# Kernel tuning notes

Measured on AMD Instinct MI355X. Metric: run time of the kernel, lower is better.

Reference implementation:

```python
import jax, jax.numpy as jnp
import numpy as np
from jax import lax

B, S, F_IN, H = 64, 512, 128, 512

def setup_inputs() -> dict:
    key = jax.random.key(0)
    ks = jax.random.split(key, 7)
    s = 1.0 / np.sqrt(H)
    return {
        "inputs": jax.random.normal(ks[0], (B, S, F_IN), dtype=jnp.float32),
        "W_ih": jax.random.normal(ks[1], (4 * H, F_IN), dtype=jnp.float32) * s,
        "W_hh": jax.random.normal(ks[2], (4 * H, H), dtype=jnp.float32) * s,
        "b_ih": jax.random.normal(ks[3], (4 * H,), dtype=jnp.float32) * s,
        "b_hh": jax.random.normal(ks[4], (4 * H,), dtype=jnp.float32) * s,
        "W_out": jax.random.normal(ks[5], (F_IN, H), dtype=jnp.float32) * s,
        "b_out": jax.random.normal(ks[6], (F_IN,), dtype=jnp.float32) * s,
    }

def reference(inputs, W_ih, W_hh, b_ih, b_hh, W_out, b_out):
    # inputs: [B, S, F]. Inference path: y=None, future=0 -> scan over all S steps.
    b, seq, _ = inputs.shape
    h = W_hh.shape[1]
    # Precompute input-to-gate projections for all timesteps: [S, B, 4H]
    x_gates = jnp.einsum("bsf,gf->sbg", inputs, W_ih) + b_ih + b_hh

    def step(carry, xg):
        h_t, c_t = carry
        gates = xg + h_t @ W_hh.T  # [B, 4H]
        i_g, f_g, g_g, o_g = jnp.split(gates, 4, axis=-1)
        i_g = jax.nn.sigmoid(i_g)
        f_g = jax.nn.sigmoid(f_g)
        g_g = jnp.tanh(g_g)
        o_g = jax.nn.sigmoid(o_g)
        c_t = f_g * c_t + i_g * g_g
        h_t = o_g * jnp.tanh(c_t)
        out = h_t @ W_out.T + b_out  # [B, F]
        return (h_t, c_t), out

    h0 = jnp.zeros((b, h), dtype=inputs.dtype)
    c0 = jnp.zeros((b, h), dtype=inputs.dtype)
    _, outs = lax.scan(step, (h0, c0), x_gates)  # outs: [S, B, F]
    return jnp.transpose(outs, (1, 0, 2))  # [B, S, F]
```

## Files before the change

### kernel.cpp

```cpp
#include <hip/hip_runtime.h>

typedef float f32x4 __attribute__((ext_vector_type(4)));

namespace {
constexpr int Bn = 64, Sn = 512, Fn = 128, Hn = 512;
constexpr int NWG = 256, NTHR = 512;
constexpr int HXS = 644;
constexpr int PQS = 581;
constexpr int RING0 = 1024;
}

__device__ __forceinline__ float sigmoid_f(float v) {
    return 1.0f / (1.0f + __expf(-v));
}
__device__ __forceinline__ float tanh_f(float v) {
    v = fminf(fmaxf(v, -15.0f), 15.0f);
    const float e = __expf(-2.0f * v);
    return (1.0f - e) / (1.0f + e);
}

__global__ __launch_bounds__(NTHR, 2)
void lstm_persist(const float* __restrict__ x,
                  const float* __restrict__ Wih,
                  const float* __restrict__ Whh,
                  const float* __restrict__ bih,
                  const float* __restrict__ bhh,
                  const float* __restrict__ Wout,
                  const float* __restrict__ bout,
                  float* __restrict__ out,
                  float* __restrict__ ws)
{
    const int w = blockIdx.x, t = threadIdx.x;
    const int xcd = w & 7, wi = w >> 3;
    const int rw = 4 * xcd + (wi & 3);
    const int bw = wi >> 2;

    const int q  = t & 31;
    const int r4 = t >> 5;
    const int k0 = 20 * q;

    const int out_fi  = (t >> 1) & 3;
    const int out_bb  = (t >> 3) & 7;
    const int out_ksl = ((t >> 6) << 1) | (t & 1);

    __shared__ float hx[8][HXS];
    __shared__ float part[32 * PQS];
    __shared__ float opart[4][8][9];
    __shared__ float gb[64];
    __shared__ float cst[16][9];
    __shared__ float bo[4];

    f32x4 wreg[4][5];
#pragma unroll
    for (int i2 = 0; i2 < 4; ++i2) {
        const int r = 4 * r4 + i2;
        const int G = (r >> 4) * Hn + rw * 16 + (r & 15);
#pragma unroll
        for (int j = 0; j < 5; ++j) {
            const int kk = k0 + 4 * j;
            const float* p = (kk < Hn) ? (Whh + (size_t)G * Hn + kk)
                                       : (Wih + (size_t)G * Fn + (kk - Hn));
            asm volatile("global_load_dwordx4 %0, %1, off"
                         : "=v"(wreg[i2][j]) : "v"(p));
        }
    }
    asm volatile("s_waitcnt vmcnt(0)");

    if (t < 64) {
        const int G = (t >> 4) * Hn + rw * 16 + (t & 15);
        gb[t] = bih[G] + bhh[G];
    }
    if (t < 4) bo[t] = bout[rw * 4 + t];
    if (t < 128) cst[t >> 3][t & 7] = 0.0f;

    unsigned* const bar = (unsigned*)ws;
    float* const ring = ws + RING0;

    if (t < 128) {
        const int ul = t & 15, bb = (t >> 4) & 7;
        float* hdst = ring + (size_t)(Bn * Hn) +
                      (size_t)(8 * bw + bb) * Hn + (16 * rw + ul);
        const float z = 0.0f;
        asm volatile("global_store_dword %0, %1, off sc0 sc1"
                     :: "v"(hdst), "v"(z) : "memory");
    }
    asm volatile("s_waitcnt vmcnt(0)" ::: "memory");
    __syncthreads();
    if (t == 0) {
        unsigned* gcnt = bar + 32 * ((w >> 4) + 1);
        const unsigned old = atomicAdd(gcnt, 1u);
        if (old == 15u) atomicAdd(bar, 1u);
        int guard = 0;
        while (__hip_atomic_load(bar, __ATOMIC_RELAXED,
                                 __HIP_MEMORY_SCOPE_AGENT) < 16u) {
            __builtin_amdgcn_s_sleep(1);
            if (++guard > 100000) break;
        }
    }
    __syncthreads();

    for (int k = 0; k <= Sn; ++k) {
        const int slot = (k & 1) ^ 1;
        const float* hsrc = ring + (size_t)slot * (Bn * Hn) + (size_t)bw * 8 * Hn;
        f32x4 v0, v1;
        {
            const float* p0 = hsrc + 4 * t;
            const float* p1 = p0 + 2048;
            asm volatile(
                "global_load_dwordx4 %0, %2, off sc0 sc1\n\t"
                "global_load_dwordx4 %1, %3, off sc0 sc1\n\t"
                "s_waitcnt vmcnt(0)"
                : "=&v"(v0), "=&v"(v1)
                : "v"(p0), "v"(p1));
        }
        {
            int fi = t;
            *(f32x4*)&hx[fi >> 7][(fi & 127) * 4] = v0;
            fi = t + 512;
            *(f32x4*)&hx[fi >> 7][(fi & 127) * 4] = v1;
        }
        if (k < Sn && t < 256) {
            const int bb = t >> 5, f4 = (t & 31) * 4;
            const f32x4 v = *(const f32x4*)(x + (size_t)(8 * bw + bb) * Sn * Fn +
                                            (size_t)k * Fn + f4);
            *(f32x4*)&hx[bb][Hn + f4] = v;
        }
        __syncthreads();

        if (k < Sn) {
            float acc[4][8];
#pragma unroll
            for (int i2 = 0; i2 < 4; ++i2)
#pragma unroll
                for (int ib = 0; ib < 8; ++ib) acc[i2][ib] = 0.0f;
#pragma unroll
            for (int j = 0; j < 5; ++j) {
                f32x4 hv[4];
#pragma unroll
                for (int ib = 0; ib < 4; ++ib)
                    hv[ib] = *(const f32x4*)&hx[ib][k0 + 4 * j];
#pragma unroll
                for (int i2 = 0; i2 < 4; ++i2)
#pragma unroll
                    for (int ib = 0; ib < 4; ++ib)
                        acc[i2][ib] += wreg[i2][j].x * hv[ib].x + wreg[i2][j].y * hv[ib].y +
                                       wreg[i2][j].z * hv[ib].z + wreg[i2][j].w * hv[ib].w;
#pragma unroll
                for (int ib = 0; ib < 4; ++ib)
                    hv[ib] = *(const f32x4*)&hx[4 + ib][k0 + 4 * j];
#pragma unroll
                for (int i2 = 0; i2 < 4; ++i2)
#pragma unroll
                    for (int ib = 0; ib < 4; ++ib)
                        acc[i2][4 + ib] += wreg[i2][j].x * hv[ib].x + wreg[i2][j].y * hv[ib].y +
                                           wreg[i2][j].z * hv[ib].z + wreg[i2][j].w * hv[ib].w;
            }
#pragma unroll
            for (int i2 = 0; i2 < 4; ++i2)
#pragma unroll
                for (int ib = 0; ib < 8; ++ib)
                    part[q * PQS + (4 * r4 + i2) * 9 + ib] = acc[i2][ib];
        }

        if (k >= 1 && t < 256) {
            const float* wo = Wout + (size_t)(rw * 4 + out_fi) * Hn + out_ksl * 64;
            const float* hrow = &hx[out_bb][out_ksl * 64];
            float oa = 0.0f;
#pragma unroll
            for (int jj = 0; jj < 16; ++jj) {
                const f32x4 wv = *(const f32x4*)(wo + 4 * jj);
                const f32x4 hv = *(const f32x4*)(hrow + 4 * jj);
                oa += wv.x * hv.x + wv.y * hv.y + wv.z * hv.z + wv.w * hv.w;
            }
            opart[out_fi][out_bb][out_ksl] = oa;
        }
        __syncthreads();

        if (k < Sn && t < 128) {
            const int ul = t & 15, bb = (t >> 4) & 7;
            float g4[4];
#pragma unroll
            for (int gate = 0; gate < 4; ++gate) {
                const int r = gate * 16 + ul;
                float s = gb[r];
#pragma unroll
                for (int qq = 0; qq < 32; ++qq) s += part[qq * PQS + r * 9 + bb];
                g4[gate] = s;
            }
            const float ig = sigmoid_f(g4[0]);
            const float fg = sigmoid_f(g4[1]);
            const float gg = tanh_f(g4[2]);
            const float og = sigmoid_f(g4[3]);
            const float cn = fg * cst[ul][bb] + ig * gg;
            cst[ul][bb] = cn;
            const float hn = og * tanh_f(cn);
            float* hdst = ring + (size_t)(k & 1) * (Bn * Hn) +
                          (size_t)(8 * bw + bb) * Hn + (16 * rw + ul);
            asm volatile("global_store_dword %0, %1, off sc0 sc1"
                         :: "v"(hdst), "v"(hn) : "memory");
        } else if (k >= 1 && t >= 128 && t < 160) {
            const int fi = (t - 128) >> 3, bb = (t - 128) & 7;
            float s = bo[fi];
#pragma unroll
            for (int qq = 0; qq < 8; ++qq) s += opart[fi][bb][qq];
            out[(size_t)(8 * bw + bb) * Sn * Fn + (size_t)(k - 1) * Fn + rw * 4 + fi] = s;
        }

        if (k < Sn) {
            asm volatile("s_waitcnt vmcnt(0)" ::: "memory");
            __syncthreads();
            if (t == 0) {
                const unsigned gen = (unsigned)(k + 2);
                unsigned* gcnt = bar + 32 * ((w >> 4) + 1);
                const unsigned old = atomicAdd(gcnt, 1u);
                if (old == 16u * gen - 1u) atomicAdd(bar, 1u);
                const unsigned target = 16u * gen;
                int guard = 0;
                while (__hip_atomic_load(bar, __ATOMIC_RELAXED,
                                         __HIP_MEMORY_SCOPE_AGENT) < target) {
                    __builtin_amdgcn_s_sleep(1);
                    if (++guard > 100000) break;
                }
            }
            __syncthreads();
        }
    }
}

extern "C" void kernel_launch(void* const* d_in, const int* in_sizes, int n_in,
                              void* d_out, int out_size, void* d_ws, size_t ws_size,
                              hipStream_t stream) {
    (void)in_sizes; (void)n_in; (void)out_size; (void)ws_size;
    const float* x    = (const float*)d_in[0];
    const float* Wih  = (const float*)d_in[1];
    const float* Whh  = (const float*)d_in[2];
    const float* bih  = (const float*)d_in[3];
    const float* bhh  = (const float*)d_in[4];
    const float* Wout = (const float*)d_in[5];
    const float* bout = (const float*)d_in[6];
    float* out = (float*)d_out;
    float* wsp = (float*)d_ws;

    hipMemsetAsync(d_ws, 0, 4096, stream);

    lstm_persist<<<dim3(NWG), dim3(NTHR), 0, stream>>>(
        x, Wih, Whh, bih, bhh, Wout, bout, out, wsp);
}
```

Before: 9.596 ms.

## Repartition LSTM across 512 workgroups of 256 threads with 8 hidden units each

Doubles the persistent workgroup count to 512 and halves threads per block to 256, so each workgroup now owns 8 hidden units (32 gate rows) instead of 16. Per-step matvec, gate reduction, output projection and barrier group sizes are remapped to match. The aim is to spread the recurrent work across more CUs and cut per-workgroup serial work on each timestep. In exchange every workgroup still reloads the full h slice for its batch group, so global traffic rises, and the grid barrier must now gather twice as many arrivals.

```diff
diff --git a/kernel.cpp b/kernel.cpp
--- a/kernel.cpp
+++ b/kernel.cpp
@@ -4,9 +4,9 @@
 
 namespace {
 constexpr int Bn = 64, Sn = 512, Fn = 128, Hn = 512;
-constexpr int NWG = 256, NTHR = 512;
+constexpr int NWG = 512, NTHR = 256;
 constexpr int HXS = 644;
-constexpr int PQS = 581;
+constexpr int PQS = 293;
 constexpr int RING0 = 1024;
 }
 
@@ -31,30 +31,30 @@
                   float* __restrict__ ws)
 {
     const int w = blockIdx.x, t = threadIdx.x;
-    const int xcd = w & 7, wi = w >> 3;
-    const int rw = 4 * xcd + (wi & 3);
-    const int bw = wi >> 2;
+    const int xcd = w & 7, wj = w >> 3;
+    const int rw = 8 * xcd + (wj & 7);
+    const int bw = wj >> 3;
 
     const int q  = t & 31;
     const int r4 = t >> 5;
     const int k0 = 20 * q;
 
-    const int out_fi  = (t >> 1) & 3;
-    const int out_bb  = (t >> 3) & 7;
-    const int out_ksl = ((t >> 6) << 1) | (t & 1);
+    const int out_fi  = t & 1;
+    const int out_bb  = (t >> 1) & 7;
+    const int out_ksl = t >> 4;
 
     __shared__ float hx[8][HXS];
     __shared__ float part[32 * PQS];
-    __shared__ float opart[4][8][9];
-    __shared__ float gb[64];
-    __shared__ float cst[16][9];
-    __shared__ float bo[4];
+    __shared__ float opart[2][8][17];
+    __shared__ float gb[32];
+    __shared__ float cst[64];
+    __shared__ float bo[2];
 
     f32x4 wreg[4][5];
 #pragma unroll
     for (int i2 = 0; i2 < 4; ++i2) {
         const int r = 4 * r4 + i2;
-        const int G = (r >> 4) * Hn + rw * 16 + (r & 15);
+        const int G = (r >> 3) * Hn + 8 * rw + (r & 7);
 #pragma unroll
         for (int j = 0; j < 5; ++j) {
             const int kk = k0 + 4 * j;
@@ -66,20 +66,20 @@
     }
     asm volatile("s_waitcnt vmcnt(0)");
 
-    if (t < 64) {
-        const int G = (t >> 4) * Hn + rw * 16 + (t & 15);
+    if (t < 32) {
+        const int G = (t >> 3) * Hn + 8 * rw + (t & 7);
         gb[t] = bih[G] + bhh[G];
     }
-    if (t < 4) bo[t] = bout[rw * 4 + t];
-    if (t < 128) cst[t >> 3][t & 7] = 0.0f;
+    if (t < 2) bo[t] = bout[rw * 2 + t];
+    if (t < 64) cst[t] = 0.0f;
 
     unsigned* const bar = (unsigned*)ws;
     float* const ring = ws + RING0;
 
-    if (t < 128) {
-        const int ul = t & 15, bb = (t >> 4) & 7;
+    if (t < 64) {
+        const int u = t & 7, bb = t >> 3;
         float* hdst = ring + (size_t)(Bn * Hn) +
-                      (size_t)(8 * bw + bb) * Hn + (16 * rw + ul);
+                      (size_t)(8 * bw + bb) * Hn + (8 * rw + u);
         const float z = 0.0f;
         asm volatile("global_store_dword %0, %1, off sc0 sc1"
                      :: "v"(hdst), "v"(z) : "memory");
@@ -87,14 +87,14 @@
     asm volatile("s_waitcnt vmcnt(0)" ::: "memory");
     __syncthreads();
     if (t == 0) {
-        unsigned* gcnt = bar + 32 * ((w >> 4) + 1);
+        unsigned* gcnt = bar + 32 * ((w >> 5) + 1);
         const unsigned old = atomicAdd(gcnt, 1u);
-        if (old == 15u) atomicAdd(bar, 1u);
+        if (old == 31u) atomicAdd(bar, 1u);
         int guard = 0;
         while (__hip_atomic_load(bar, __ATOMIC_RELAXED,
                                  __HIP_MEMORY_SCOPE_AGENT) < 16u) {
             __builtin_amdgcn_s_sleep(1);
-            if (++guard > 100000) break;
+            if (++guard > 200000) break;
         }
     }
     __syncthreads();
@@ -102,24 +102,32 @@
     for (int k = 0; k <= Sn; ++k) {
         const int slot = (k & 1) ^ 1;
         const float* hsrc = ring + (size_t)slot * (Bn * Hn) + (size_t)bw * 8 * Hn;
-        f32x4 v0, v1;
+        f32x4 v0, v1, v2, v3;
         {
             const float* p0 = hsrc + 4 * t;
-            const float* p1 = p0 + 2048;
+            const float* p1 = p0 + 1024;
+            const float* p2 = p0 + 2048;
+            const float* p3 = p0 + 3072;
             asm volatile(
-                "global_load_dwordx4 %0, %2, off sc0 sc1\n\t"
-                "global_load_dwordx4 %1, %3, off sc0 sc1\n\t"
+                "global_load_dwordx4 %0, %4, off sc0 sc1\n\t"
+                "global_load_dwordx4 %1, %5, off sc0 sc1\n\t"
+                "global_load_dwordx4 %2, %6, off sc0 sc1\n\t"
+                "global_load_dwordx4 %3, %7, off sc0 sc1\n\t"
                 "s_waitcnt vmcnt(0)"
-                : "=&v"(v0), "=&v"(v1)
-                : "v"(p0), "v"(p1));
+                : "=&v"(v0), "=&v"(v1), "=&v"(v2), "=&v"(v3)
+                : "v"(p0), "v"(p1), "v"(p2), "v"(p3));
         }
         {
             int fi = t;
             *(f32x4*)&hx[fi >> 7][(fi & 127) * 4] = v0;
+            fi = t + 256;
+            *(f32x4*)&hx[fi >> 7][(fi & 127) * 4] = v1;
             fi = t + 512;
-            *(f32x4*)&hx[fi >> 7][(fi & 127) * 4] = v1;
-        }
-        if (k < Sn && t < 256) {
+            *(f32x4*)&hx[fi >> 7][(fi & 127) * 4] = v2;
+            fi = t + 768;
+            *(f32x4*)&hx[fi >> 7][(fi & 127) * 4] = v3;
+        }
+        if (k < Sn) {
             const int bb = t >> 5, f4 = (t & 31) * 4;
             const f32x4 v = *(const f32x4*)(x + (size_t)(8 * bw + bb) * Sn * Fn +
                                             (size_t)k * Fn + f4);
@@ -162,12 +170,12 @@
                     part[q * PQS + (4 * r4 + i2) * 9 + ib] = acc[i2][ib];
         }
 
-        if (k >= 1 && t < 256) {
-            const float* wo = Wout + (size_t)(rw * 4 + out_fi) * Hn + out_ksl * 64;
-            const float* hrow = &hx[out_bb][out_ksl * 64];
+        if (k >= 1) {
+            const float* wo = Wout + (size_t)(rw * 2 + out_fi) * Hn + out_ksl * 32;
+            const float* hrow = &hx[out_bb][out_ksl * 32];
             float oa = 0.0f;
 #pragma unroll
-            for (int jj = 0; jj < 16; ++jj) {
+            for (int jj = 0; jj < 8; ++jj) {
                 const f32x4 wv = *(const f32x4*)(wo + 4 * jj);
                 const f32x4 hv = *(const f32x4*)(hrow + 4 * jj);
                 oa += wv.x * hv.x + wv.y * hv.y + wv.z * hv.z + wv.w * hv.w;
@@ -176,12 +184,12 @@
         }
         __syncthreads();
 
-        if (k < Sn && t < 128) {
-            const int ul = t & 15, bb = (t >> 4) & 7;
+        if (k < Sn && t < 64) {
+            const int u = t & 7, bb = t >> 3;
             float g4[4];
 #pragma unroll
             for (int gate = 0; gate < 4; ++gate) {
-                const int r = gate * 16 + ul;
+                const int r = gate * 8 + u;
                 float s = gb[r];
 #pragma unroll
                 for (int qq = 0; qq < 32; ++qq) s += part[qq * PQS + r * 9 + bb];
@@ -191,19 +199,19 @@
             const float fg = sigmoid_f(g4[1]);
             const float gg = tanh_f(g4[2]);
             const float og = sigmoid_f(g4[3]);
-            const float cn = fg * cst[ul][bb] + ig * gg;
-            cst[ul][bb] = cn;
+            const float cn = fg * cst[t] + ig * gg;
+            cst[t] = cn;
             const float hn = og * tanh_f(cn);
             float* hdst = ring + (size_t)(k & 1) * (Bn * Hn) +
-                          (size_t)(8 * bw + bb) * Hn + (16 * rw + ul);
+                          (size_t)(8 * bw + bb) * Hn + (8 * rw + u);
             asm volatile("global_store_dword %0, %1, off sc0 sc1"
                          :: "v"(hdst), "v"(hn) : "memory");
-        } else if (k >= 1 && t >= 128 && t < 160) {
-            const int fi = (t - 128) >> 3, bb = (t - 128) & 7;
+        } else if (k >= 1 && t >= 64 && t < 80) {
+            const int fi = (t - 64) & 1, bb = (t - 64) >> 1;
             float s = bo[fi];
 #pragma unroll
-            for (int qq = 0; qq < 8; ++qq) s += opart[fi][bb][qq];
-            out[(size_t)(8 * bw + bb) * Sn * Fn + (size_t)(k - 1) * Fn + rw * 4 + fi] = s;
+            for (int qq = 0; qq < 16; ++qq) s += opart[fi][bb][qq];
+            out[(size_t)(8 * bw + bb) * Sn * Fn + (size_t)(k - 1) * Fn + rw * 2 + fi] = s;
         }
 
         if (k < Sn) {
@@ -211,15 +219,15 @@
             __syncthreads();
             if (t == 0) {
                 const unsigned gen = (unsigned)(k + 2);
-                unsigned* gcnt = bar + 32 * ((w >> 4) + 1);
+                unsigned* gcnt = bar + 32 * ((w >> 5) + 1);
                 const unsigned old = atomicAdd(gcnt, 1u);
-                if (old == 16u * gen - 1u) atomicAdd(bar, 1u);
+                if (old == 32u * gen - 1u) atomicAdd(bar, 1u);
                 const unsigned target = 16u * gen;
                 int guard = 0;
                 while (__hip_atomic_load(bar, __ATOMIC_RELAXED,
                                          __HIP_MEMORY_SCOPE_AGENT) < target) {
                     __builtin_amdgcn_s_sleep(1);
-                    if (++guard > 100000) break;
+                    if (++guard > 200000) break;
                 }
             }
             __syncthreads();
```

Measured after the change: 9.979 ms. +4.0%, slower.
